# Kernel optimization log

Measured on AMD Instinct MI355X. Metric: run time of the kernel, lower is better.

## Reference

```python
import jax, jax.numpy as jnp
import numpy as np

B, N_IN, N_H, N_OUT = 128, 256, 256, 256


def _bimul(W, X):
    # MatrixBiMul: bilinear map W X W^T, W: [out, in], X: [b, in, in] -> [b, out, out]
    return jnp.einsum('oi,bij,qj->boq', W, X, W)


def setup_inputs() -> dict:
    key = jax.random.key(0)
    ks = jax.random.split(key, 12)
    s_in = 1.0 / np.sqrt(N_IN)
    s_h = 1.0 / np.sqrt(N_H)
    return {
        'input': jax.random.normal(ks[0], (B, N_IN, N_IN), jnp.float32),
        'hidden': jax.random.normal(ks[1], (B, N_H, N_H), jnp.float32),
        'cell': jax.random.normal(ks[2], (B, N_H, N_H), jnp.float32),
        'W_fx': jax.random.normal(ks[3], (N_H, N_IN), jnp.float32) * s_in,
        'W_ix': jax.random.normal(ks[4], (N_H, N_IN), jnp.float32) * s_in,
        'W_ox': jax.random.normal(ks[5], (N_OUT, N_IN), jnp.float32) * s_in,
        'W_gx': jax.random.normal(ks[6], (N_H, N_IN), jnp.float32) * s_in,
        'W_fh': jax.random.normal(ks[7], (N_H, N_H), jnp.float32) * s_h,
        'W_ih': jax.random.normal(ks[8], (N_H, N_H), jnp.float32) * s_h,
        'W_oh': jax.random.normal(ks[9], (N_OUT, N_H), jnp.float32) * s_h,
        'W_gh': jax.random.normal(ks[10], (N_H, N_H), jnp.float32) * s_h,
        'W_oc': jax.random.normal(ks[11], (N_OUT, N_H), jnp.float32) * s_h,
    }


def reference(input, hidden, cell, W_fx, W_ix, W_ox, W_gx, W_fh, W_ih, W_oh, W_gh, W_oc):
    fgate = jax.nn.relu(_bimul(W_fx, input) + _bimul(W_fh, hidden))
    igate = jax.nn.relu(_bimul(W_ix, input) + _bimul(W_ih, hidden))
    ogate = jax.nn.relu(_bimul(W_ox, input) + _bimul(W_oh, hidden))
    ggate = jax.nn.relu(_bimul(W_gx, input) + _bimul(W_gh, hidden))
    c = fgate + cell + igate + ggate  # note: additive, as in source (not fgate*cell)
    h = ogate + jax.nn.relu(_bimul(W_oc, c))
    return (h, c)
```

## Files before the change

kernel.cpp:

```cpp
#include <hip/hip_runtime.h>

typedef __bf16 bf16x8 __attribute__((ext_vector_type(8)));
typedef float f32x4 __attribute__((ext_vector_type(4)));

__device__ __forceinline__ unsigned short f2bf(float f) {
    unsigned int u = __builtin_bit_cast(unsigned int, f);
    u += 0x7fff + ((u >> 16) & 1);
    return (unsigned short)(u >> 16);
}

__device__ __forceinline__ void stage_pair(
    const unsigned short* __restrict__ Ap, int lda,
    const unsigned short* __restrict__ Bp, int ldb,
    unsigned short* lds, int k0, int tid)
{
#pragma unroll
    for (int it = 0; it < 4; ++it) {
        int li = it * 256 + tid;
        int row = li >> 3;
        int sc = ((li & 7) ^ (row & 7)) * 8;
        __builtin_amdgcn_global_load_lds(
            (const __attribute__((address_space(1))) void*)(Ap + (long)row * lda + k0 + sc),
            (__attribute__((address_space(3))) void*)&lds[li * 8], 16, 0, 0);
        __builtin_amdgcn_global_load_lds(
            (const __attribute__((address_space(1))) void*)(Bp + (long)row * ldb + k0 + sc),
            (__attribute__((address_space(3))) void*)&lds[8192 + li * 8], 16, 0, 0);
    }
}

__device__ __forceinline__ void compute_tile(
    const unsigned short* lds, int lane, int wm, int wn, f32x4 (&acc)[4][4])
{
#pragma unroll
    for (int kk = 0; kk < 2; ++kk) {
        const int cl = kk * 4 + (lane >> 4);
        bf16x8 af[4], bfr[4];
#pragma unroll
        for (int m = 0; m < 4; ++m) {
            int row = wm + m * 16 + (lane & 15);
            af[m] = *(const bf16x8*)&lds[row * 64 + ((cl ^ (row & 7)) * 8)];
        }
#pragma unroll
        for (int n = 0; n < 4; ++n) {
            int row = wn + n * 16 + (lane & 15);
            bfr[n] = *(const bf16x8*)&lds[8192 + row * 64 + ((cl ^ (row & 7)) * 8)];
        }
#pragma unroll
        for (int m = 0; m < 4; ++m)
#pragma unroll
            for (int n = 0; n < 4; ++n)
                acc[m][n] = __builtin_amdgcn_mfma_f32_16x16x32_bf16(af[m], bfr[n], acc[m][n], 0, 0, 0);
    }
}

__global__ __launch_bounds__(256)
void cvt_weights(const float* __restrict__ fx, const float* __restrict__ ix,
                 const float* __restrict__ ox, const float* __restrict__ gx,
                 const float* __restrict__ fh, const float* __restrict__ ih,
                 const float* __restrict__ oh, const float* __restrict__ gh,
                 const float* __restrict__ oc,
                 unsigned short* __restrict__ Wcat, unsigned short* __restrict__ Wocb)
{
    int idx = blockIdx.x * 256 + threadIdx.x;
    if (idx < 524288) {
        int g = idx >> 17;
        int rem = idx & 131071;
        int q = rem >> 9;
        int j = rem & 511;
        const float* xs = (g == 0) ? fx : (g == 1) ? ix : (g == 2) ? ox : gx;
        const float* hs = (g == 0) ? fh : (g == 1) ? ih : (g == 2) ? oh : gh;
        float v = (j < 256) ? xs[q * 256 + j] : hs[q * 256 + (j - 256)];
        Wcat[idx] = f2bf(v);
    } else if (idx < 589824) {
        int k = idx - 524288;
        Wocb[k] = f2bf(oc[k]);
    }
}

template <int MODE>
__global__ __launch_bounds__(256)
void gemm_stage1(const float* __restrict__ Xf, const float* __restrict__ Hf,
                 const unsigned short* __restrict__ Wb,
                 unsigned short* __restrict__ Tout)
{
    __shared__ alignas(16) unsigned short lds[32768];

    const int tid = threadIdx.x;
    const int lane = tid & 63;
    const int w = tid >> 6;

    int d = blockIdx.x + 4 * blockIdx.y + 512 * blockIdx.z;
    int swz = (MODE == 0) ? ((d & 7) * 512 + (d >> 3))
                          : ((d & 7) * 64 + (d >> 3));
    const int x = swz & 3;
    const int b = (swz >> 2) & 127;
    const int gz = (MODE == 0) ? (swz >> 9) : 0;
    const int g = gz >> 1, hf = gz & 1;
    const int ti = (x & 1) * 128;
    const int tq = (x >> 1) * 128;
    const int wm = (w >> 1) * 64;
    const int wn = (w & 1) * 64;
    const int ldb = (MODE == 0) ? 512 : 256;

    const float* Ap = ((MODE == 0) ? (hf ? Hf : Xf) : Xf) + (long)b * 65536 + (long)ti * 256;
    const unsigned short* Bp = (MODE == 0)
        ? Wb + (long)g * 131072 + (long)tq * 512 + hf * 256
        : Wb + (long)tq * 256;

    f32x4 acc[4][4];
#pragma unroll
    for (int m = 0; m < 4; ++m)
#pragma unroll
        for (int n = 0; n < 4; ++n)
            acc[m][n] = (f32x4){0.f, 0.f, 0.f, 0.f};

    float4 pre[4][2];
#pragma unroll
    for (int it = 0; it < 4; ++it) {
        int li = it * 256 + tid;
        int row = li >> 3;
        int ck = li & 7;
        const float* ga = Ap + (long)row * 256 + ck * 8;
        pre[it][0] = *(const float4*)ga;
        pre[it][1] = *(const float4*)(ga + 4);
    }
#pragma unroll
    for (int it = 0; it < 4; ++it) {
        int li = it * 256 + tid;
        int row = li >> 3;
        int sc = ((li & 7) ^ (row & 7)) * 8;
        __builtin_amdgcn_global_load_lds(
            (const __attribute__((address_space(1))) void*)(Bp + (long)row * ldb + sc),
            (__attribute__((address_space(3))) void*)&lds[8192 + li * 8], 16, 0, 0);
    }

#pragma unroll
    for (int t = 0; t < 4; ++t) {
        unsigned short* buf = lds + (t & 1) * 16384;
#pragma unroll
        for (int it = 0; it < 4; ++it) {
            int li = it * 256 + tid;
            int row = li >> 3;
            int ck = li & 7;
            const float* pf = (const float*)&pre[it][0];
            uint4 uv;
            uv.x = (unsigned)f2bf(pf[0]) | ((unsigned)f2bf(pf[1]) << 16);
            uv.y = (unsigned)f2bf(pf[2]) | ((unsigned)f2bf(pf[3]) << 16);
            uv.z = (unsigned)f2bf(pf[4]) | ((unsigned)f2bf(pf[5]) << 16);
            uv.w = (unsigned)f2bf(pf[6]) | ((unsigned)f2bf(pf[7]) << 16);
            *(uint4*)&buf[row * 64 + ((ck ^ (row & 7)) * 8)] = uv;
        }
        __syncthreads();
        if (t < 3) {
            unsigned short* nbuf = lds + ((t + 1) & 1) * 16384;
#pragma unroll
            for (int it = 0; it < 4; ++it) {
                int li = it * 256 + tid;
                int row = li >> 3;
                int ck = li & 7;
                const float* ga = Ap + (long)row * 256 + (t + 1) * 64 + ck * 8;
                pre[it][0] = *(const float4*)ga;
                pre[it][1] = *(const float4*)(ga + 4);
            }
#pragma unroll
            for (int it = 0; it < 4; ++it) {
                int li = it * 256 + tid;
                int row = li >> 3;
                int sc = ((li & 7) ^ (row & 7)) * 8;
                __builtin_amdgcn_global_load_lds(
                    (const __attribute__((address_space(1))) void*)(Bp + (long)row * ldb + (t + 1) * 64 + sc),
                    (__attribute__((address_space(3))) void*)&nbuf[8192 + li * 8], 16, 0, 0);
            }
        }
        compute_tile(buf, lane, wm, wn, acc);
    }

    __syncthreads();
    unsigned short (*ldsT)[136] = (unsigned short(*)[136])lds;
    const int r0 = (lane >> 4) * 4;
    const int c0 = lane & 15;
#pragma unroll
    for (int m = 0; m < 4; ++m)
#pragma unroll
        for (int n = 0; n < 4; ++n)
#pragma unroll
            for (int r = 0; r < 4; ++r) {
                int row = wm + m * 16 + r0 + r;
                int col = wn + n * 16 + c0;
                ldsT[col][row] = f2bf(acc[m][n][r]);
            }
    __syncthreads();
    unsigned short* Cb;
    int ldc;
    if (MODE == 0) { Cb = Tout + (long)g * 16777216 + (long)b * 131072 + hf * 256; ldc = 512; }
    else           { Cb = Tout + (long)b * 65536; ldc = 256; }
#pragma unroll
    for (int it = 0; it < 8; ++it) {
        int idx = it * 256 + tid;
        int qq = idx >> 4;
        int ch = idx & 15;
        uint4 v = *(const uint4*)&ldsT[qq][ch * 8];
        *(uint4*)&Cb[(long)(tq + qq) * ldc + ti + ch * 8] = v;
    }
}

__global__ __launch_bounds__(256)
void gemm_gateB(const unsigned short* __restrict__ Tcat,
                const unsigned short* __restrict__ Wcat,
                const float* __restrict__ cell,
                float* __restrict__ out_c, float* __restrict__ out_h)
{
    __shared__ alignas(16) unsigned short lds[32768];

    const int tid = threadIdx.x;
    const int lane = tid & 63;
    const int w = tid >> 6;

    int orig = blockIdx.x + 4 * blockIdx.y;
    int swz = (orig & 7) * 64 + (orig >> 3);
    const int x = swz & 3;
    const int b = swz >> 2;
    const int to = (x >> 1) * 128;
    const int tq = (x & 1) * 128;
    const int wm = (w >> 1) * 64;
    const int wn = (w & 1) * 64;

    f32x4 accc[4][4], acc[4][4];
#pragma unroll
    for (int m = 0; m < 4; ++m)
#pragma unroll
        for (int n = 0; n < 4; ++n) {
            accc[m][n] = (f32x4){0.f, 0.f, 0.f, 0.f};
            acc[m][n] = (f32x4){0.f, 0.f, 0.f, 0.f};
        }

    {
        const unsigned short* Ap0 = Wcat + (long)to * 512;
        const unsigned short* Bp0 = Tcat + (long)b * 131072 + (long)tq * 512;
        stage_pair(Ap0, 512, Bp0, 512, lds, 0, tid);
    }
    for (int u = 0; u < 32; ++u) {
        __syncthreads();
        if (u + 1 < 32) {
            int s = (u + 1) >> 3;
            int gv = s ^ (s >> 1);
            const unsigned short* Ap = Wcat + (long)gv * 131072 + (long)to * 512;
            const unsigned short* Bp = Tcat + (long)gv * 16777216 + (long)b * 131072 + (long)tq * 512;
            stage_pair(Ap, 512, Bp, 512, lds + ((u + 1) & 1) * 16384, ((u + 1) & 7) * 64, tid);
        }
        compute_tile(lds + (u & 1) * 16384, lane, wm, wn, acc);
        if ((u & 7) == 7 && u != 31) {
#pragma unroll
            for (int m = 0; m < 4; ++m)
#pragma unroll
                for (int n = 0; n < 4; ++n)
#pragma unroll
                    for (int r = 0; r < 4; ++r) {
                        float v = acc[m][n][r];
                        accc[m][n][r] += (v > 0.f ? v : 0.f);
                        acc[m][n][r] = 0.f;
                    }
        }
    }

    const float* cb = cell + (long)b * 65536;
    float* co = out_c + (long)b * 65536;
    float* ho = out_h + (long)b * 65536;
    const int r0 = (lane >> 4) * 4;
    const int c0 = lane & 15;
#pragma unroll
    for (int m = 0; m < 4; ++m)
#pragma unroll
        for (int n = 0; n < 4; ++n)
#pragma unroll
            for (int r = 0; r < 4; ++r) {
                int row = to + wm + m * 16 + r0 + r;
                int col = tq + wn + n * 16 + c0;
                long idx = (long)row * 256 + col;
                co[idx] = accc[m][n][r] + cb[idx];
                float v = acc[m][n][r];
                ho[idx] = (v > 0.f ? v : 0.f);
            }
}

__global__ __launch_bounds__(256)
void gemm_hfinal(const unsigned short* __restrict__ Wocb,
                 const unsigned short* __restrict__ ScT,
                 float* __restrict__ out_h)
{
    __shared__ alignas(16) unsigned short lds[32768];

    const int tid = threadIdx.x;
    const int lane = tid & 63;
    const int w = tid >> 6;

    int orig = blockIdx.x + 4 * blockIdx.y;
    int swz = (orig & 7) * 64 + (orig >> 3);
    const int x = swz & 3;
    const int b = swz >> 2;
    const int to = (x >> 1) * 128;
    const int tq = (x & 1) * 128;
    const int wm = (w >> 1) * 64;
    const int wn = (w & 1) * 64;

    const unsigned short* Ap = Wocb + (long)to * 256;
    const unsigned short* Bp = ScT + (long)b * 65536 + (long)tq * 256;

    f32x4 acc[4][4];
#pragma unroll
    for (int m = 0; m < 4; ++m)
#pragma unroll
        for (int n = 0; n < 4; ++n)
            acc[m][n] = (f32x4){0.f, 0.f, 0.f, 0.f};

    stage_pair(Ap, 256, Bp, 256, lds, 0, tid);
#pragma unroll
    for (int t = 0; t < 4; ++t) {
        __syncthreads();
        if (t + 1 < 4)
            stage_pair(Ap, 256, Bp, 256, lds + ((t + 1) & 1) * 16384, (t + 1) * 64, tid);
        compute_tile(lds + (t & 1) * 16384, lane, wm, wn, acc);
    }

    float* ho = out_h + (long)b * 65536;
    const int r0 = (lane >> 4) * 4;
    const int c0 = lane & 15;
#pragma unroll
    for (int m = 0; m < 4; ++m)
#pragma unroll
        for (int n = 0; n < 4; ++n)
#pragma unroll
            for (int r = 0; r < 4; ++r) {
                int row = to + wm + m * 16 + r0 + r;
                int col = tq + wn + n * 16 + c0;
                float v = acc[m][n][r];
                ho[(long)row * 256 + col] += (v > 0.f ? v : 0.f);
            }
}

extern "C" void kernel_launch(void* const* d_in, const int* in_sizes, int n_in,
                              void* d_out, int out_size, void* d_ws, size_t ws_size,
                              hipStream_t stream)
{
    (void)in_sizes; (void)n_in; (void)out_size; (void)ws_size;

    const float* X    = (const float*)d_in[0];
    const float* H    = (const float*)d_in[1];
    const float* cell = (const float*)d_in[2];
    const float* Wxp[4] = {(const float*)d_in[3], (const float*)d_in[4],
                           (const float*)d_in[5], (const float*)d_in[6]};
    const float* Whp[4] = {(const float*)d_in[7], (const float*)d_in[8],
                           (const float*)d_in[9], (const float*)d_in[10]};
    const float* Wocf = (const float*)d_in[11];

    float* out_h = (float*)d_out;
    float* out_c = out_h + 8388608;

    unsigned short* ws   = (unsigned short*)d_ws;
    unsigned short* ScT  = ws;
    unsigned short* Wcat = ws + 16777216;
    unsigned short* Wocb = ws + 17301504;
    unsigned short* Tcat = ws + 17367040;

    cvt_weights<<<dim3(2304), 256, 0, stream>>>(Wxp[0], Wxp[1], Wxp[2], Wxp[3],
                                                Whp[0], Whp[1], Whp[2], Whp[3],
                                                Wocf, Wcat, Wocb);
    gemm_stage1<0><<<dim3(4, 128, 8), 256, 0, stream>>>(X, H, Wcat, Tcat);
    gemm_gateB<<<dim3(4, 128), 256, 0, stream>>>(Tcat, Wcat, cell, out_c, out_h);
    gemm_stage1<1><<<dim3(4, 128, 1), 256, 0, stream>>>(out_c, nullptr, Wocb, ScT);
    gemm_hfinal<<<dim3(4, 128), 256, 0, stream>>>(Wocb, ScT, out_h);
}
```

Before: 205.1 us.

## Pre-convert X/H to bf16 and restructure stage-1 GEMMs around bf16 operands

Adds a separate pass that converts input and hidden to bf16 once. The first-stage GEMM now streams both operands straight into LDS with async global-to-LDS loads. It runs single-buffered with no register fp32 prefetch, and swaps operand roles so it writes Tcat directly without an LDS transpose. The gate kernel also emits a bf16 copy of c, which feeds a generic NT GEMM used for both W_oc bimul stages. This removes in-kernel conversion work, at the cost of extra full-tensor bf16 traffic, lost double buffering in stage 1, and scattered 2-byte epilogue stores.

```diff
diff --git a/kernel.cpp b/kernel.cpp
--- a/kernel.cpp
+++ b/kernel.cpp
@@ -51,6 +51,22 @@
             for (int n = 0; n < 4; ++n)
                 acc[m][n] = __builtin_amdgcn_mfma_f32_16x16x32_bf16(af[m], bfr[n], acc[m][n], 0, 0, 0);
     }
+}
+
+__global__ __launch_bounds__(256)
+void cvt_xh(const float* __restrict__ X, const float* __restrict__ H,
+            unsigned short* __restrict__ XHb)
+{
+    long e = (long)(blockIdx.x * 256 + threadIdx.x) * 8;
+    const float* s = (e < 8388608) ? (X + e) : (H + (e - 8388608));
+    float4 a = *(const float4*)s;
+    float4 c = *(const float4*)(s + 4);
+    uint4 uv;
+    uv.x = (unsigned)f2bf(a.x) | ((unsigned)f2bf(a.y) << 16);
+    uv.y = (unsigned)f2bf(a.z) | ((unsigned)f2bf(a.w) << 16);
+    uv.z = (unsigned)f2bf(c.x) | ((unsigned)f2bf(c.y) << 16);
+    uv.w = (unsigned)f2bf(c.z) | ((unsigned)f2bf(c.w) << 16);
+    *(uint4*)&XHb[e] = uv;
 }
 
 __global__ __launch_bounds__(256)
@@ -77,35 +93,30 @@
     }
 }
 
-template <int MODE>
-__global__ __launch_bounds__(256)
-void gemm_stage1(const float* __restrict__ Xf, const float* __restrict__ Hf,
-                 const unsigned short* __restrict__ Wb,
-                 unsigned short* __restrict__ Tout)
-{
-    __shared__ alignas(16) unsigned short lds[32768];
+__global__ __launch_bounds__(256)
+void gemm_s1(const unsigned short* __restrict__ Wcat,
+             const unsigned short* __restrict__ XHb,
+             unsigned short* __restrict__ Tcat)
+{
+    __shared__ alignas(16) unsigned short lds[16384];
 
     const int tid = threadIdx.x;
     const int lane = tid & 63;
     const int w = tid >> 6;
 
     int d = blockIdx.x + 4 * blockIdx.y + 512 * blockIdx.z;
-    int swz = (MODE == 0) ? ((d & 7) * 512 + (d >> 3))
-                          : ((d & 7) * 64 + (d >> 3));
+    int swz = (d & 7) * 512 + (d >> 3);
     const int x = swz & 3;
     const int b = (swz >> 2) & 127;
-    const int gz = (MODE == 0) ? (swz >> 9) : 0;
+    const int gz = swz >> 9;
     const int g = gz >> 1, hf = gz & 1;
+    const int tq = (x >> 1) * 128;
     const int ti = (x & 1) * 128;
-    const int tq = (x >> 1) * 128;
     const int wm = (w >> 1) * 64;
     const int wn = (w & 1) * 64;
-    const int ldb = (MODE == 0) ? 512 : 256;
-
-    const float* Ap = ((MODE == 0) ? (hf ? Hf : Xf) : Xf) + (long)b * 65536 + (long)ti * 256;
-    const unsigned short* Bp = (MODE == 0)
-        ? Wb + (long)g * 131072 + (long)tq * 512 + hf * 256
-        : Wb + (long)tq * 256;
+
+    const unsigned short* Ap = Wcat + (long)g * 131072 + (long)tq * 512 + hf * 256;
+    const unsigned short* Bp = XHb + (long)hf * 8388608 + (long)b * 65536 + (long)ti * 256;
 
     f32x4 acc[4][4];
 #pragma unroll
@@ -114,69 +125,15 @@
         for (int n = 0; n < 4; ++n)
             acc[m][n] = (f32x4){0.f, 0.f, 0.f, 0.f};
 
-    float4 pre[4][2];
-#pragma unroll
-    for (int it = 0; it < 4; ++it) {
-        int li = it * 256 + tid;
-        int row = li >> 3;
-        int ck = li & 7;
-        const float* ga = Ap + (long)row * 256 + ck * 8;
-        pre[it][0] = *(const float4*)ga;
-        pre[it][1] = *(const float4*)(ga + 4);
-    }
-#pragma unroll
-    for (int it = 0; it < 4; ++it) {
-        int li = it * 256 + tid;
-        int row = li >> 3;
-        int sc = ((li & 7) ^ (row & 7)) * 8;
-        __builtin_amdgcn_global_load_lds(
-            (const __attribute__((address_space(1))) void*)(Bp + (long)row * ldb + sc),
-            (__attribute__((address_space(3))) void*)&lds[8192 + li * 8], 16, 0, 0);
-    }
-
 #pragma unroll
     for (int t = 0; t < 4; ++t) {
-        unsigned short* buf = lds + (t & 1) * 16384;
-#pragma unroll
-        for (int it = 0; it < 4; ++it) {
-            int li = it * 256 + tid;
-            int row = li >> 3;
-            int ck = li & 7;
-            const float* pf = (const float*)&pre[it][0];
-            uint4 uv;
-            uv.x = (unsigned)f2bf(pf[0]) | ((unsigned)f2bf(pf[1]) << 16);
-            uv.y = (unsigned)f2bf(pf[2]) | ((unsigned)f2bf(pf[3]) << 16);
-            uv.z = (unsigned)f2bf(pf[4]) | ((unsigned)f2bf(pf[5]) << 16);
-            uv.w = (unsigned)f2bf(pf[6]) | ((unsigned)f2bf(pf[7]) << 16);
-            *(uint4*)&buf[row * 64 + ((ck ^ (row & 7)) * 8)] = uv;
-        }
+        if (t > 0) __syncthreads();
+        stage_pair(Ap, 512, Bp, 256, lds, t * 64, tid);
         __syncthreads();
-        if (t < 3) {
-            unsigned short* nbuf = lds + ((t + 1) & 1) * 16384;
-#pragma unroll
-            for (int it = 0; it < 4; ++it) {
-                int li = it * 256 + tid;
-                int row = li >> 3;
-                int ck = li & 7;
-                const float* ga = Ap + (long)row * 256 + (t + 1) * 64 + ck * 8;
-                pre[it][0] = *(const float4*)ga;
-                pre[it][1] = *(const float4*)(ga + 4);
-            }
-#pragma unroll
-            for (int it = 0; it < 4; ++it) {
-                int li = it * 256 + tid;
-                int row = li >> 3;
-                int sc = ((li & 7) ^ (row & 7)) * 8;
-                __builtin_amdgcn_global_load_lds(
-                    (const __attribute__((address_space(1))) void*)(Bp + (long)row * ldb + (t + 1) * 64 + sc),
-                    (__attribute__((address_space(3))) void*)&nbuf[8192 + li * 8], 16, 0, 0);
-            }
-        }
-        compute_tile(buf, lane, wm, wn, acc);
-    }
-
-    __syncthreads();
-    unsigned short (*ldsT)[136] = (unsigned short(*)[136])lds;
+        compute_tile(lds, lane, wm, wn, acc);
+    }
+
+    unsigned short* Cb = Tcat + (long)g * 16777216 + (long)b * 131072 + hf * 256;
     const int r0 = (lane >> 4) * 4;
     const int c0 = lane & 15;
 #pragma unroll
@@ -185,30 +142,18 @@
         for (int n = 0; n < 4; ++n)
 #pragma unroll
             for (int r = 0; r < 4; ++r) {
-                int row = wm + m * 16 + r0 + r;
-                int col = wn + n * 16 + c0;
-                ldsT[col][row] = f2bf(acc[m][n][r]);
+                int row = tq + wm + m * 16 + r0 + r;
+                int col = ti + wn + n * 16 + c0;
+                Cb[(long)row * 512 + col] = f2bf(acc[m][n][r]);
             }
-    __syncthreads();
-    unsigned short* Cb;
-    int ldc;
-    if (MODE == 0) { Cb = Tout + (long)g * 16777216 + (long)b * 131072 + hf * 256; ldc = 512; }
-    else           { Cb = Tout + (long)b * 65536; ldc = 256; }
-#pragma unroll
-    for (int it = 0; it < 8; ++it) {
-        int idx = it * 256 + tid;
-        int qq = idx >> 4;
-        int ch = idx & 15;
-        uint4 v = *(const uint4*)&ldsT[qq][ch * 8];
-        *(uint4*)&Cb[(long)(tq + qq) * ldc + ti + ch * 8] = v;
-    }
 }
 
 __global__ __launch_bounds__(256)
 void gemm_gateB(const unsigned short* __restrict__ Tcat,
                 const unsigned short* __restrict__ Wcat,
                 const float* __restrict__ cell,
-                float* __restrict__ out_c, float* __restrict__ out_h)
+                float* __restrict__ out_c, float* __restrict__ out_h,
+                unsigned short* __restrict__ cb16)
 {
     __shared__ alignas(16) unsigned short lds[32768];
 
@@ -266,6 +211,7 @@
     const float* cb = cell + (long)b * 65536;
     float* co = out_c + (long)b * 65536;
     float* ho = out_h + (long)b * 65536;
+    unsigned short* cbo = cb16 + (long)b * 65536;
     const int r0 = (lane >> 4) * 4;
     const int c0 = lane & 15;
 #pragma unroll
@@ -277,16 +223,19 @@
                 int row = to + wm + m * 16 + r0 + r;
                 int col = tq + wn + n * 16 + c0;
                 long idx = (long)row * 256 + col;
-                co[idx] = accc[m][n][r] + cb[idx];
+                float cv = accc[m][n][r] + cb[idx];
+                co[idx] = cv;
+                cbo[idx] = f2bf(cv);
                 float v = acc[m][n][r];
                 ho[idx] = (v > 0.f ? v : 0.f);
             }
 }
 
-__global__ __launch_bounds__(256)
-void gemm_hfinal(const unsigned short* __restrict__ Wocb,
-                 const unsigned short* __restrict__ ScT,
-                 float* __restrict__ out_h)
+template <int MODE>
+__global__ __launch_bounds__(256)
+void gemm_nt2(const unsigned short* __restrict__ A, int lda, long sAy,
+              const unsigned short* __restrict__ B, int ldb, long sBy,
+              void* __restrict__ Cv, int ldc, long sCy)
 {
     __shared__ alignas(16) unsigned short lds[32768];
 
@@ -298,13 +247,13 @@
     int swz = (orig & 7) * 64 + (orig >> 3);
     const int x = swz & 3;
     const int b = swz >> 2;
-    const int to = (x >> 1) * 128;
-    const int tq = (x & 1) * 128;
+    const int tm = (x >> 1) * 128;
+    const int tn = (x & 1) * 128;
     const int wm = (w >> 1) * 64;
     const int wn = (w & 1) * 64;
 
-    const unsigned short* Ap = Wocb + (long)to * 256;
-    const unsigned short* Bp = ScT + (long)b * 65536 + (long)tq * 256;
+    const unsigned short* Ap = A + b * sAy + (long)tm * lda;
+    const unsigned short* Bp = B + b * sBy + (long)tn * ldb;
 
     f32x4 acc[4][4];
 #pragma unroll
@@ -313,29 +262,46 @@
         for (int n = 0; n < 4; ++n)
             acc[m][n] = (f32x4){0.f, 0.f, 0.f, 0.f};
 
-    stage_pair(Ap, 256, Bp, 256, lds, 0, tid);
+    stage_pair(Ap, lda, Bp, ldb, lds, 0, tid);
 #pragma unroll
     for (int t = 0; t < 4; ++t) {
         __syncthreads();
         if (t + 1 < 4)
-            stage_pair(Ap, 256, Bp, 256, lds + ((t + 1) & 1) * 16384, (t + 1) * 64, tid);
+            stage_pair(Ap, lda, Bp, ldb, lds + ((t + 1) & 1) * 16384, (t + 1) * 64, tid);
         compute_tile(lds + (t & 1) * 16384, lane, wm, wn, acc);
     }
 
-    float* ho = out_h + (long)b * 65536;
+    const long coff = b * sCy;
     const int r0 = (lane >> 4) * 4;
     const int c0 = lane & 15;
-#pragma unroll
-    for (int m = 0; m < 4; ++m)
-#pragma unroll
-        for (int n = 0; n < 4; ++n)
-#pragma unroll
-            for (int r = 0; r < 4; ++r) {
-                int row = to + wm + m * 16 + r0 + r;
-                int col = tq + wn + n * 16 + c0;
-                float v = acc[m][n][r];
-                ho[(long)row * 256 + col] += (v > 0.f ? v : 0.f);
-            }
+
+    if (MODE == 0) {
+        unsigned short* C = (unsigned short*)Cv + coff;
+#pragma unroll
+        for (int m = 0; m < 4; ++m)
+#pragma unroll
+            for (int n = 0; n < 4; ++n)
+#pragma unroll
+                for (int r = 0; r < 4; ++r) {
+                    int row = tm + wm + m * 16 + r0 + r;
+                    int col = tn + wn + n * 16 + c0;
+                    C[(long)row * ldc + col] = f2bf(acc[m][n][r]);
+                }
+    } else {
+        float* C = (float*)Cv + coff;
+#pragma unroll
+        for (int m = 0; m < 4; ++m)
+#pragma unroll
+            for (int n = 0; n < 4; ++n)
+#pragma unroll
+                for (int r = 0; r < 4; ++r) {
+                    int row = tm + wm + m * 16 + r0 + r;
+                    int col = tn + wn + n * 16 + c0;
+                    long idx = (long)row * ldc + col;
+                    float v = acc[m][n][r];
+                    C[idx] += (v > 0.f ? v : 0.f);
+                }
+    }
 }
 
 extern "C" void kernel_launch(void* const* d_in, const int* in_sizes, int n_in,
@@ -357,16 +323,23 @@
     float* out_c = out_h + 8388608;
 
     unsigned short* ws   = (unsigned short*)d_ws;
-    unsigned short* ScT  = ws;
+    unsigned short* XHb  = ws;
     unsigned short* Wcat = ws + 16777216;
     unsigned short* Wocb = ws + 17301504;
     unsigned short* Tcat = ws + 17367040;
-
+    unsigned short* cb16 = ws + 84475904;
+    unsigned short* ScT  = ws + 92864512;
+
+    cvt_xh<<<dim3(8192), 256, 0, stream>>>(X, H, XHb);
     cvt_weights<<<dim3(2304), 256, 0, stream>>>(Wxp[0], Wxp[1], Wxp[2], Wxp[3],
                                                 Whp[0], Whp[1], Whp[2], Whp[3],
                                                 Wocf, Wcat, Wocb);
-    gemm_stage1<0><<<dim3(4, 128, 8), 256, 0, stream>>>(X, H, Wcat, Tcat);
-    gemm_gateB<<<dim3(4, 128), 256, 0, stream>>>(Tcat, Wcat, cell, out_c, out_h);
-    gemm_stage1<1><<<dim3(4, 128, 1), 256, 0, stream>>>(out_c, nullptr, Wocb, ScT);
-    gemm_hfinal<<<dim3(4, 128), 256, 0, stream>>>(Wocb, ScT, out_h);
-}
+    gemm_s1<<<dim3(4, 128, 8), 256, 0, stream>>>(Wcat, XHb, Tcat);
+    gemm_gateB<<<dim3(4, 128), 256, 0, stream>>>(Tcat, Wcat, cell, out_c, out_h, cb16);
+    gemm_nt2<0><<<dim3(4, 128), 256, 0, stream>>>(
+        Wocb, 256, 0L, cb16, 256, 65536L,
+        (void*)ScT, 256, 65536L);
+    gemm_nt2<2><<<dim3(4, 128), 256, 0, stream>>>(
+        Wocb, 256, 0L, ScT, 256, 65536L,
+        (void*)out_h, 256, 65536L);
+}
```

Measured after the change: 193.4 us. 1.06x faster.
